# Optimization experiments

Hardware: AMD Instinct MI355X
Metric: run time of the kernel (lower is better)

The kernel has to match this reference:

```python
import jax, jax.numpy as jnp
import numpy as np

B, V, TG = 512, 16, 48
LAB, MED, GLU, E = 256, 192, 16, 64


def _attn_enc(x, W1, b1, Wq, Wk):
    # Attn_encoder: project then self-attend; out [..., L, H]
    h = jnp.tanh(x @ W1 + b1)
    q, k = h @ Wq, h @ Wk
    a = jax.nn.softmax(jnp.einsum('...qd,...kd->...qk', q, k) / jnp.sqrt(jnp.float32(Wq.shape[1])), axis=-1)
    return a @ h


def _mha(q, k, v, Wq, Wk, Wv, Wo, H=4):
    # module's MHA: output length follows v (v acts as query side)
    d = Wq.shape[1]; dh = d // H
    qh = (v @ Wq).reshape(v.shape[:-1] + (H, dh))
    kh = (k @ Wk).reshape(k.shape[:-1] + (H, dh))
    vh = (q @ Wv).reshape(q.shape[:-1] + (H, dh))
    a = jax.nn.softmax(jnp.einsum('...qhd,...khd->...hqk', qh, kh) / jnp.sqrt(jnp.float32(dh)), axis=-1)
    o = jnp.einsum('...hqk,...khd->...qhd', a, vh)
    return o.reshape(o.shape[:-2] + (d,)) @ Wo


def _forward(lab, glu, time, med, ehr_adj, ddi_adj, time_adj,
             Ws1, bs1, Ws2, bs2, Wl1, bl1, Wl2, bl2, Wl3, bl3,
             Wm1, bm1, Wmq, Wmk, Wg1, bg1, Wgq, Wgk,
             gru_Wx, gru_Wh, gru_b,
             m1_Wq, m1_Wk, m1_Wv, m1_Wo, m2_Wq, m2_Wk, m2_Wv, m2_Wo,
             Wo1, bo1, Wo2, bo2):
    Bn, Vn, Tn = glu.shape
    G = gru_Wh.shape[0]
    # static_ll: [B, E//2] repeated over visits
    s = jax.nn.relu(lab @ Ws1 + bs1)
    s = jax.nn.relu(s @ Ws2 + bs2)
    static_fea = jnp.broadcast_to(s[:, None, :], (Bn, Vn, s.shape[-1]))
    # glu_encoder: GRU over per-visit glucose/time readings -> [B, V, GLU]
    x = jnp.stack([glu, time], -1).reshape(Bn * Vn, Tn, 2)
    xs = jnp.swapaxes(x, 0, 1)  # [T, BV, 2]
    def step(h, xt):
        g = xt @ gru_Wx + gru_b
        gh = h @ gru_Wh
        z = jax.nn.sigmoid(g[:, :G] + gh[:, :G])
        r = jax.nn.sigmoid(g[:, G:2 * G] + gh[:, G:2 * G])
        n = jnp.tanh(g[:, 2 * G:] + r * gh[:, 2 * G:])
        return (1.0 - z) * n + z * h, None
    hT, _ = jax.lax.scan(step, jnp.zeros((Bn * Vn, G), glu.dtype), xs)
    glu_enc = hT.reshape(Bn, Vn, G)
    glu_rep = _attn_enc(glu_enc, Wg1, bg1, Wgq, Wgk)        # [B, V, E//2]
    patient_rep = jnp.concatenate([glu_rep, static_fea], -1)  # [B, V, E]
    med_rep = _attn_enc(med[:, :-1, :], Wm1, bm1, Wmq, Wmk)   # [B, V-1, E]
    # drug memory from graph adjacencies (shared across patients)
    drug_mem = (ehr_adj @ Wl1 + bl1) + (time_adj @ Wl2 + bl2) - (ddi_adj @ Wl3 + bl3)  # [MED, E]
    E_en = _mha(patient_rep, patient_rep, med_rep, m1_Wq, m1_Wk, m1_Wv, m1_Wo)  # [B, V-1, E]
    dm = jnp.broadcast_to(drug_mem, (Bn,) + drug_mem.shape)
    E_de = _mha(E_en, E_en, dm, m2_Wq, m2_Wk, m2_Wv, m2_Wo)   # [B, MED, E]
    final = E_de.reshape(Bn, -1)
    o = jax.nn.relu(final)
    o = jax.nn.relu(o @ Wo1 + bo1)
    return o @ Wo2 + bo2  # [B, MED]


def setup_inputs() -> dict:
    ks = iter(jax.random.split(jax.random.key(0), 64))
    def nrm(shape, s=0.05):
        return jax.random.normal(next(ks), shape, dtype=jnp.float32) * s
    z = lambda *shape: jnp.zeros(shape, jnp.float32)
    d = {}
    d['lab'] = jax.random.normal(next(ks), (B, LAB), dtype=jnp.float32)
    d['glu'] = jax.random.normal(next(ks), (B, V, TG), dtype=jnp.float32)
    d['time'] = jax.random.uniform(next(ks), (B, V, TG), dtype=jnp.float32)
    d['med'] = jax.random.uniform(next(ks), (B, V, MED), dtype=jnp.float32)
    d['ehr_adj'] = jax.random.uniform(next(ks), (MED, MED), dtype=jnp.float32)
    d['ddi_adj'] = jax.random.uniform(next(ks), (MED, MED), dtype=jnp.float32)
    d['time_adj'] = jax.random.uniform(next(ks), (MED, MED), dtype=jnp.float32)
    d['Ws1'] = nrm((LAB, E)); d['bs1'] = z(E)
    d['Ws2'] = nrm((E, E // 2)); d['bs2'] = z(E // 2)
    d['Wl1'] = nrm((MED, E)); d['bl1'] = z(E)
    d['Wl2'] = nrm((MED, E)); d['bl2'] = z(E)
    d['Wl3'] = nrm((MED, E)); d['bl3'] = z(E)
    d['Wm1'] = nrm((MED, E)); d['bm1'] = z(E)
    d['Wmq'] = nrm((E, E // 2)); d['Wmk'] = nrm((E, E // 2))
    d['Wg1'] = nrm((GLU, E // 2)); d['bg1'] = z(E // 2)
    d['Wgq'] = nrm((E // 2, E // 4)); d['Wgk'] = nrm((E // 2, E // 4))
    d['gru_Wx'] = nrm((2, 3 * GLU)); d['gru_Wh'] = nrm((GLU, 3 * GLU)); d['gru_b'] = z(3 * GLU)
    for p in ['m1', 'm2']:
        for w in ['Wq', 'Wk', 'Wv', 'Wo']:
            d[p + '_' + w] = nrm((E, E))
    d['Wo1'] = nrm((E * MED, E * MED // 8)); d['bo1'] = z(E * MED // 8)
    d['Wo2'] = nrm((E * MED // 8, MED)); d['bo2'] = z(MED)
    return d


def reference(lab, glu, time, med, ehr_adj, ddi_adj, time_adj,
              Ws1, bs1, Ws2, bs2, Wl1, bl1, Wl2, bl2, Wl3, bl3,
              Wm1, bm1, Wmq, Wmk, Wg1, bg1, Wgq, Wgk,
              gru_Wx, gru_Wh, gru_b,
              m1_Wq, m1_Wk, m1_Wv, m1_Wo, m2_Wq, m2_Wk, m2_Wv, m2_Wo,
              Wo1, bo1, Wo2, bo2):
    return _forward(lab, glu, time, med, ehr_adj, ddi_adj, time_adj,
                    Ws1, bs1, Ws2, bs2, Wl1, bl1, Wl2, bl2, Wl3, bl3,
                    Wm1, bm1, Wmq, Wmk, Wg1, bg1, Wgq, Wgk,
                    gru_Wx, gru_Wh, gru_b,
                    m1_Wq, m1_Wk, m1_Wv, m1_Wo, m2_Wq, m2_Wk, m2_Wv, m2_Wo,
                    Wo1, bo1, Wo2, bo2)
```

## Files before the change

kernel.cpp:

```cpp
#include <hip/hip_runtime.h>
#include <math.h>

#define DEVINL __device__ __forceinline__

DEVINL float sigm(float x) { return 1.0f / (1.0f + __expf(-x)); }
DEVINL float tanh_fast(float x) { return 2.0f / (1.0f + __expf(-2.0f * x)) - 1.0f; }
DEVINL unsigned short bf16rne(float f) {
    unsigned u = __float_as_uint(f);
    return (unsigned short)((u + 0x7FFFu + ((u >> 16) & 1u)) >> 16);
}

typedef __attribute__((ext_vector_type(8))) short bf16x8;
typedef __attribute__((ext_vector_type(4))) float f32x4;

__global__ void gemm_small(const float* __restrict__ A, const float* __restrict__ W,
                           const float* __restrict__ bias, float* __restrict__ C,
                           int M, int N, int K, int act, int vgroup)
{
    int idx = blockIdx.x * blockDim.x + threadIdx.x;
    if (idx >= M * N) return;
    int m = idx / N, n = idx - m * N;
    int am = m;
    if (vgroup) { int g = m / vgroup; am = g * (vgroup + 1) + (m - g * vgroup); }
    const float* a = A + (size_t)am * K;
    const float* w = W + n;
    float acc = bias ? bias[n] : 0.0f;
    for (int k = 0; k < K; k += 4) {
        float4 av = *(const float4*)&a[k];
        float w0 = w[(size_t)k * N];
        float w1 = w[(size_t)(k + 1) * N];
        float w2 = w[(size_t)(k + 2) * N];
        float w3 = w[(size_t)(k + 3) * N];
        acc = fmaf(av.x, w0, acc);
        acc = fmaf(av.y, w1, acc);
        acc = fmaf(av.z, w2, acc);
        acc = fmaf(av.w, w3, acc);
    }
    if (act == 1) acc = fmaxf(acc, 0.0f);
    else if (act == 2) acc = tanh_fast(acc);
    C[idx] = acc;
}

__global__ __launch_bounds__(256) void gru_wave(const float* __restrict__ glu,
    const float* __restrict__ timev, const float* __restrict__ Wx,
    const float* __restrict__ Wh, const float* __restrict__ bb,
    float* __restrict__ out)
{
    __shared__ float sWh[768], sWx[96], sb[48];
    int tid = threadIdx.x;
    for (int i = tid; i < 768; i += 256) sWh[i] = Wh[i];
    if (tid < 96) sWx[tid] = Wx[tid];
    if (tid < 48) sb[tid] = bb[tid];
    __syncthreads();
    int j = tid & 15;
    int seq = blockIdx.x * 16 + (tid >> 4);
    int gbase = (tid & 63) & 0x30;
    float whz[16], whr[16], whn[16];
#pragma unroll
    for (int i = 0; i < 16; ++i) {
        whz[i] = sWh[i * 48 + j];
        whr[i] = sWh[i * 48 + 16 + j];
        whn[i] = sWh[i * 48 + 32 + j];
    }
    float wxz0 = sWx[j],      wxr0 = sWx[16 + j], wxn0 = sWx[32 + j];
    float wxz1 = sWx[48 + j], wxr1 = sWx[64 + j], wxn1 = sWx[80 + j];
    float bz = sb[j], br = sb[16 + j], bn = sb[32 + j];
    const float* gp = glu + (size_t)seq * 48;
    const float* tp = timev + (size_t)seq * 48;
    float h = 0.0f;
    for (int t = 0; t < 48; ++t) {
        float gl = gp[t], tm = tp[t];
        float gz = fmaf(gl, wxz0, fmaf(tm, wxz1, bz));
        float gr = fmaf(gl, wxr0, fmaf(tm, wxr1, br));
        float gn = fmaf(gl, wxn0, fmaf(tm, wxn1, bn));
        float ghn = 0.0f;
#pragma unroll
        for (int i = 0; i < 16; ++i) {
            float hb = __shfl(h, gbase + i, 64);
            gz = fmaf(hb, whz[i], gz);
            gr = fmaf(hb, whr[i], gr);
            ghn = fmaf(hb, whn[i], ghn);
        }
        float z = sigm(gz), r = sigm(gr);
        float n = tanh_fast(gn + r * ghn);
        h = (1.0f - z) * n + z * h;
    }
    out[(size_t)seq * 16 + j] = h;
}

__global__ __launch_bounds__(256) void glu_attn(const float* __restrict__ hg,
    const float* __restrict__ Wq, const float* __restrict__ Wk,
    const float* __restrict__ s2, float* __restrict__ patient)
{
    int b = blockIdx.x, tid = threadIdx.x;
    __shared__ float sh[512], sq[256], sk[256], ss[256];
    sh[tid] = hg[(size_t)b * 512 + tid];
    sh[256 + tid] = hg[(size_t)b * 512 + 256 + tid];
    __syncthreads();
    {
        int p = tid >> 4, j = tid & 15;
        float aq = 0.0f, ak = 0.0f;
        for (int i = 0; i < 32; ++i) {
            float hv = sh[p * 32 + i];
            aq = fmaf(hv, Wq[i * 16 + j], aq);
            ak = fmaf(hv, Wk[i * 16 + j], ak);
        }
        sq[tid] = aq; sk[tid] = ak;
    }
    __syncthreads();
    {
        int p = tid >> 4, pk = tid & 15;
        float a = 0.0f;
        for (int j = 0; j < 16; ++j) a = fmaf(sq[p * 16 + j], sk[pk * 16 + j], a);
        ss[tid] = a * 0.25f;
    }
    __syncthreads();
    if (tid < 16) {
        float mx = -1e30f;
        for (int k = 0; k < 16; ++k) mx = fmaxf(mx, ss[tid * 16 + k]);
        float sum = 0.0f;
        for (int k = 0; k < 16; ++k) { float e = __expf(ss[tid * 16 + k] - mx); ss[tid * 16 + k] = e; sum += e; }
        float inv = 1.0f / sum;
        for (int k = 0; k < 16; ++k) ss[tid * 16 + k] *= inv;
    }
    __syncthreads();
    for (int o = tid; o < 512; o += 256) {
        int p = o >> 5, c = o & 31;
        float acc = 0.0f;
        for (int pk = 0; pk < 16; ++pk) acc = fmaf(ss[p * 16 + pk], sh[pk * 32 + c], acc);
        patient[((size_t)b * 16 + p) * 64 + c] = acc;
        patient[((size_t)b * 16 + p) * 64 + 32 + c] = s2[(size_t)b * 32 + c];
    }
}

__global__ __launch_bounds__(256) void med_attn(const float* __restrict__ hm,
    const float* __restrict__ Wq, const float* __restrict__ Wk,
    float* __restrict__ med_rep)
{
    int b = blockIdx.x, tid = threadIdx.x;
    __shared__ float sh[960], sq[480], sk[480], ss[225];
    for (int i = tid; i < 960; i += 256) sh[i] = hm[(size_t)b * 960 + i];
    __syncthreads();
    for (int o = tid; o < 480; o += 256) {
        int p = o >> 5, j = o & 31;
        float aq = 0.0f, ak = 0.0f;
        for (int i = 0; i < 64; ++i) {
            float hv = sh[p * 64 + i];
            aq = fmaf(hv, Wq[i * 32 + j], aq);
            ak = fmaf(hv, Wk[i * 32 + j], ak);
        }
        sq[o] = aq; sk[o] = ak;
    }
    __syncthreads();
    if (tid < 225) {
        int p = tid / 15, pk = tid - p * 15;
        float a = 0.0f;
        for (int j = 0; j < 32; ++j) a = fmaf(sq[p * 32 + j], sk[pk * 32 + j], a);
        ss[tid] = a * 0.17677669529663687f;
    }
    __syncthreads();
    if (tid < 15) {
        float mx = -1e30f;
        for (int k = 0; k < 15; ++k) mx = fmaxf(mx, ss[tid * 15 + k]);
        float sum = 0.0f;
        for (int k = 0; k < 15; ++k) { float e = __expf(ss[tid * 15 + k] - mx); ss[tid * 15 + k] = e; sum += e; }
        float inv = 1.0f / sum;
        for (int k = 0; k < 15; ++k) ss[tid * 15 + k] *= inv;
    }
    __syncthreads();
    for (int o = tid; o < 960; o += 256) {
        int p = o >> 6, c = o & 63;
        float acc = 0.0f;
        for (int pk = 0; pk < 15; ++pk) acc = fmaf(ss[p * 15 + pk], sh[pk * 64 + c], acc);
        med_rep[(size_t)b * 960 + o] = acc;
    }
}

__global__ void drugmem_kernel(const float* __restrict__ ehr, const float* __restrict__ tadj,
    const float* __restrict__ ddi,
    const float* __restrict__ Wl1, const float* __restrict__ bl1,
    const float* __restrict__ Wl2, const float* __restrict__ bl2,
    const float* __restrict__ Wl3, const float* __restrict__ bl3,
    float* __restrict__ dm)
{
    int idx = blockIdx.x * 256 + threadIdx.x;
    if (idx >= 192 * 64) return;
    int m = idx >> 6, n = idx & 63;
    float acc = bl1[n] + bl2[n] - bl3[n];
    for (int k = 0; k < 192; ++k) {
        acc = fmaf(ehr[m * 192 + k], Wl1[k * 64 + n], acc);
        acc = fmaf(tadj[m * 192 + k], Wl2[k * 64 + n], acc);
        acc = fmaf(-ddi[m * 192 + k], Wl3[k * 64 + n], acc);
    }
    dm[idx] = acc;
}

__global__ __launch_bounds__(256) void mha1_attn(const float* __restrict__ qh1,
    const float* __restrict__ kh1, const float* __restrict__ vh1,
    const float* __restrict__ Wo, float* __restrict__ Een)
{
    int b = blockIdx.x, tid = threadIdx.x;
    __shared__ float sq[1020], sk[1088], sv[1024], ss[960], so[960];
    for (int i = tid; i < 960; i += 256) sq[(i >> 6) * 68 + (i & 63)] = qh1[(size_t)b * 960 + i];
    for (int i = tid; i < 1024; i += 256) {
        sk[(i >> 6) * 68 + (i & 63)] = kh1[(size_t)b * 1024 + i];
        sv[i] = vh1[(size_t)b * 1024 + i];
    }
    __syncthreads();
    for (int o = tid; o < 960; o += 256) {
        int hh = o / 240, rem = o - hh * 240, q = rem >> 4, k = rem & 15;
        float a = 0.0f;
        for (int d = 0; d < 16; ++d) a = fmaf(sq[q * 68 + hh * 16 + d], sk[k * 68 + hh * 16 + d], a);
        ss[o] = a * 0.25f;
    }
    __syncthreads();
    if (tid < 60) {
        int base = tid * 16;
        float mx = -1e30f;
        for (int k = 0; k < 16; ++k) mx = fmaxf(mx, ss[base + k]);
        float sum = 0.0f;
        for (int k = 0; k < 16; ++k) { float e = __expf(ss[base + k] - mx); ss[base + k] = e; sum += e; }
        float inv = 1.0f / sum;
        for (int k = 0; k < 16; ++k) ss[base + k] *= inv;
    }
    __syncthreads();
    for (int o = tid; o < 960; o += 256) {
        int q = o >> 6, j = o & 63, hh = j >> 4;
        float a = 0.0f;
        for (int k = 0; k < 16; ++k) a = fmaf(ss[hh * 240 + q * 16 + k], sv[k * 64 + j], a);
        so[o] = a;
    }
    __syncthreads();
    for (int o = tid; o < 960; o += 256) {
        int q = o >> 6, c = o & 63;
        float a = 0.0f;
        for (int j = 0; j < 64; ++j) a = fmaf(so[q * 64 + j], Wo[j * 64 + c], a);
        Een[(size_t)b * 960 + o] = a;
    }
}

__global__ __launch_bounds__(256) void mha2_attn2(const float* __restrict__ qh2,
    const float* __restrict__ kh2, const float* __restrict__ vh2,
    float* __restrict__ so_all)
{
    int b = blockIdx.x >> 2, q0 = (blockIdx.x & 3) * 48;
    int tid = threadIdx.x;
    __shared__ float skp[1020], sv[960], ss[2880];
    for (int i = tid; i < 960; i += 256) {
        skp[(i >> 6) * 68 + (i & 63)] = kh2[(size_t)b * 960 + i];
        sv[i] = vh2[(size_t)b * 960 + i];
    }
    __syncthreads();
    for (int o = tid; o < 2880; o += 256) {
        int hh = o / 720, rem = o - hh * 720, q = rem / 15, k = rem - q * 15;
        const float* qp = qh2 + (size_t)(q0 + q) * 64 + hh * 16;
        float a = 0.0f;
        for (int d = 0; d < 16; ++d) a = fmaf(qp[d], skp[k * 68 + hh * 16 + d], a);
        ss[o] = a * 0.25f;
    }
    __syncthreads();
    if (tid < 192) {
        int hh = tid / 48, q = tid - hh * 48;
        int base = hh * 720 + q * 15;
        float mx = -1e30f;
        for (int k = 0; k < 15; ++k) mx = fmaxf(mx, ss[base + k]);
        float sum = 0.0f;
        for (int k = 0; k < 15; ++k) { float e = __expf(ss[base + k] - mx); ss[base + k] = e; sum += e; }
        float inv = 1.0f / sum;
        for (int k = 0; k < 15; ++k) ss[base + k] *= inv;
    }
    __syncthreads();
    for (int o = tid; o < 3072; o += 256) {
        int q = o >> 6, j = o & 63, hh = j >> 4;
        float a = 0.0f;
        for (int k = 0; k < 15; ++k) a = fmaf(ss[hh * 720 + q * 15 + k], sv[k * 64 + j], a);
        so_all[((size_t)b * 192 + q0 + q) * 64 + j] = a;
    }
}

__global__ __launch_bounds__(256) void gemm64_relu_bf16(const float* __restrict__ A,
    const float* __restrict__ B, unsigned short* __restrict__ Obf)
{
    __shared__ float As[64 * 20];
    __shared__ float Bs[16 * 64];
    int tid = threadIdx.x;
    int m0 = blockIdx.x * 64;
    float acc[4][4] = {};
    int arow = tid >> 2, akq = (tid & 3) << 2;
    int brow = tid >> 4, bnq = (tid & 15) << 2;
    int tm0 = (tid >> 4) << 2, tn0 = (tid & 15) << 2;
    for (int kt = 0; kt < 64; kt += 16) {
        float4 av = *(const float4*)&A[(size_t)(m0 + arow) * 64 + kt + akq];
        *(float4*)&As[arow * 20 + akq] = av;
        float4 bv = *(const float4*)&B[(size_t)(kt + brow) * 64 + bnq];
        *(float4*)&Bs[brow * 64 + bnq] = bv;
        __syncthreads();
#pragma unroll
        for (int kk = 0; kk < 16; ++kk) {
            float4 b4 = *(const float4*)&Bs[kk * 64 + tn0];
            float a0 = As[(tm0 + 0) * 20 + kk];
            float a1 = As[(tm0 + 1) * 20 + kk];
            float a2 = As[(tm0 + 2) * 20 + kk];
            float a3 = As[(tm0 + 3) * 20 + kk];
            acc[0][0] = fmaf(a0, b4.x, acc[0][0]); acc[0][1] = fmaf(a0, b4.y, acc[0][1]);
            acc[0][2] = fmaf(a0, b4.z, acc[0][2]); acc[0][3] = fmaf(a0, b4.w, acc[0][3]);
            acc[1][0] = fmaf(a1, b4.x, acc[1][0]); acc[1][1] = fmaf(a1, b4.y, acc[1][1]);
            acc[1][2] = fmaf(a1, b4.z, acc[1][2]); acc[1][3] = fmaf(a1, b4.w, acc[1][3]);
            acc[2][0] = fmaf(a2, b4.x, acc[2][0]); acc[2][1] = fmaf(a2, b4.y, acc[2][1]);
            acc[2][2] = fmaf(a2, b4.z, acc[2][2]); acc[2][3] = fmaf(a2, b4.w, acc[2][3]);
            acc[3][0] = fmaf(a3, b4.x, acc[3][0]); acc[3][1] = fmaf(a3, b4.y, acc[3][1]);
            acc[3][2] = fmaf(a3, b4.z, acc[3][2]); acc[3][3] = fmaf(a3, b4.w, acc[3][3]);
        }
        __syncthreads();
    }
#pragma unroll
    for (int i = 0; i < 4; ++i) {
        unsigned r0 = (unsigned)bf16rne(fmaxf(acc[i][0], 0.f)) | ((unsigned)bf16rne(fmaxf(acc[i][1], 0.f)) << 16);
        unsigned r1 = (unsigned)bf16rne(fmaxf(acc[i][2], 0.f)) | ((unsigned)bf16rne(fmaxf(acc[i][3], 0.f)) << 16);
        uint2 v = { r0, r1 };
        *(uint2*)&Obf[(size_t)(m0 + tm0 + i) * 64 + tn0] = v;
    }
}

__global__ __launch_bounds__(256) void gemm_mfma_bf16(
    const unsigned short* __restrict__ Abf, const float* __restrict__ B,
    float* __restrict__ Cp, int M, int N, int K, int klen)
{
    __shared__ unsigned short As[64 * 64];
    __shared__ unsigned short Bs[64 * 64];
    int tid = threadIdx.x;
    int lane = tid & 63, wid = tid >> 6;
    int wr = wid >> 1, wc = wid & 1;
    int n0 = blockIdx.x * 64, m0 = blockIdx.y * 64;
    int kbase0 = blockIdx.z * klen;
    f32x4 acc[2][2] = {};

    int bn = tid & 63, bkc = (tid >> 6) * 16;
    for (int kt = 0; kt < klen; kt += 64) {
        int kb = kbase0 + kt;
#pragma unroll
        for (int c = 0; c < 2; ++c) {
            int ch = tid + c * 256;
            int row = ch >> 3, kc0 = (ch & 7) << 3;
            uint4 v = *(const uint4*)&Abf[(size_t)(m0 + row) * K + kb + kc0];
            int bo = ((row << 7) + (kc0 << 1)) ^ ((row & 7) << 4);
            *(uint4*)((char*)As + bo) = v;
        }
        {
            const float* bp = &B[(size_t)(kb + bkc) * N + n0 + bn];
#pragma unroll
            for (int j = 0; j < 16; j += 2) {
                float f0 = bp[(size_t)j * N];
                float f1 = bp[(size_t)(j + 1) * N];
                unsigned u = (unsigned)bf16rne(f0) | ((unsigned)bf16rne(f1) << 16);
                int k = bkc + j;
                int bo = ((bn << 7) + (k << 1)) ^ ((bn & 7) << 4);
                *(unsigned*)((char*)Bs + bo) = u;
            }
        }
        __syncthreads();
#pragma unroll
        for (int kk = 0; kk < 64; kk += 32) {
            int kb2 = (kk + ((lane >> 4) << 3)) << 1;
            bf16x8 af[2], bfg[2];
#pragma unroll
            for (int fm = 0; fm < 2; ++fm) {
                int row = (wr << 5) + (fm << 4) + (lane & 15);
                af[fm] = *(const bf16x8*)((const char*)As + (((row << 7) + kb2) ^ ((row & 7) << 4)));
            }
#pragma unroll
            for (int fn = 0; fn < 2; ++fn) {
                int col = (wc << 5) + (fn << 4) + (lane & 15);
                bfg[fn] = *(const bf16x8*)((const char*)Bs + (((col << 7) + kb2) ^ ((col & 7) << 4)));
            }
#pragma unroll
            for (int fm = 0; fm < 2; ++fm)
#pragma unroll
                for (int fn = 0; fn < 2; ++fn)
                    acc[fm][fn] = __builtin_amdgcn_mfma_f32_16x16x32_bf16(af[fm], bfg[fn], acc[fm][fn], 0, 0, 0);
        }
        __syncthreads();
    }
    float* cp = Cp + (size_t)blockIdx.z * M * N;
#pragma unroll
    for (int fm = 0; fm < 2; ++fm)
#pragma unroll
        for (int fn = 0; fn < 2; ++fn) {
            int row = m0 + (wr << 5) + (fm << 4) + ((lane >> 4) << 2);
            int col = n0 + (wc << 5) + (fn << 4) + (lane & 15);
#pragma unroll
            for (int r = 0; r < 4; ++r)
                cp[(size_t)(row + r) * N + col] = acc[fm][fn][r];
        }
}

template <int RELU_A>
__global__ __launch_bounds__(256) void gemm_sk(const float* __restrict__ A,
    const float* __restrict__ B, float* __restrict__ Cp,
    int M, int N, int K, int klen)
{
    __shared__ float As[64 * 20];
    __shared__ float Bs[16 * 64];
    int tid = threadIdx.x;
    int n0 = blockIdx.x * 64, m0 = blockIdx.y * 64;
    int bs = blockIdx.z;
    int kbase0 = bs * klen;
    float acc[4][4] = {};
    int arow = tid >> 2, akq = (tid & 3) << 2;
    int brow = tid >> 4, bnq = (tid & 15) << 2;
    int tm0 = (tid >> 4) << 2, tn0 = (tid & 15) << 2;
    for (int kt = 0; kt < klen; kt += 16) {
        int kb = kbase0 + kt;
        float4 av = *(const float4*)&A[(size_t)(m0 + arow) * K + kb + akq];
        if (RELU_A) {
            av.x = fmaxf(av.x, 0.0f); av.y = fmaxf(av.y, 0.0f);
            av.z = fmaxf(av.z, 0.0f); av.w = fmaxf(av.w, 0.0f);
        }
        *(float4*)&As[arow * 20 + akq] = av;
        float4 bv = *(const float4*)&B[(size_t)(kb + brow) * N + n0 + bnq];
        *(float4*)&Bs[brow * 64 + bnq] = bv;
        __syncthreads();
#pragma unroll
        for (int kk = 0; kk < 16; ++kk) {
            float4 b4 = *(const float4*)&Bs[kk * 64 + tn0];
            float a0 = As[(tm0 + 0) * 20 + kk];
            float a1 = As[(tm0 + 1) * 20 + kk];
            float a2 = As[(tm0 + 2) * 20 + kk];
            float a3 = As[(tm0 + 3) * 20 + kk];
            acc[0][0] = fmaf(a0, b4.x, acc[0][0]); acc[0][1] = fmaf(a0, b4.y, acc[0][1]);
            acc[0][2] = fmaf(a0, b4.z, acc[0][2]); acc[0][3] = fmaf(a0, b4.w, acc[0][3]);
            acc[1][0] = fmaf(a1, b4.x, acc[1][0]); acc[1][1] = fmaf(a1, b4.y, acc[1][1]);
            acc[1][2] = fmaf(a1, b4.z, acc[1][2]); acc[1][3] = fmaf(a1, b4.w, acc[1][3]);
            acc[2][0] = fmaf(a2, b4.x, acc[2][0]); acc[2][1] = fmaf(a2, b4.y, acc[2][1]);
            acc[2][2] = fmaf(a2, b4.z, acc[2][2]); acc[2][3] = fmaf(a2, b4.w, acc[2][3]);
            acc[3][0] = fmaf(a3, b4.x, acc[3][0]); acc[3][1] = fmaf(a3, b4.y, acc[3][1]);
            acc[3][2] = fmaf(a3, b4.z, acc[3][2]); acc[3][3] = fmaf(a3, b4.w, acc[3][3]);
        }
        __syncthreads();
    }
    float* cp = Cp + (size_t)bs * M * N;
#pragma unroll
    for (int i = 0; i < 4; ++i)
#pragma unroll
        for (int j = 0; j < 4; ++j)
            cp[(size_t)(m0 + tm0 + i) * N + n0 + tn0 + j] = acc[i][j];
}

__global__ void reduce_bias_act(const float* __restrict__ part, const float* __restrict__ bias,
                                float* __restrict__ out, int MN, int N, int S, int relu)
{
    int idx = blockIdx.x * 256 + threadIdx.x;
    if (idx >= MN) return;
    float a = bias[idx % N];
    for (int s = 0; s < S; ++s) a += part[(size_t)s * MN + idx];
    if (relu) a = fmaxf(a, 0.0f);
    out[idx] = a;
}

extern "C" void kernel_launch(void* const* d_in, const int* in_sizes, int n_in,
                              void* d_out, int out_size, void* d_ws, size_t ws_size,
                              hipStream_t stream)
{
    const float* lab    = (const float*)d_in[0];
    const float* glu    = (const float*)d_in[1];
    const float* timev  = (const float*)d_in[2];
    const float* med    = (const float*)d_in[3];
    const float* ehr    = (const float*)d_in[4];
    const float* ddi    = (const float*)d_in[5];
    const float* tadj   = (const float*)d_in[6];
    const float* Ws1    = (const float*)d_in[7];
    const float* bs1    = (const float*)d_in[8];
    const float* Ws2    = (const float*)d_in[9];
    const float* bs2    = (const float*)d_in[10];
    const float* Wl1    = (const float*)d_in[11];
    const float* bl1    = (const float*)d_in[12];
    const float* Wl2    = (const float*)d_in[13];
    const float* bl2    = (const float*)d_in[14];
    const float* Wl3    = (const float*)d_in[15];
    const float* bl3    = (const float*)d_in[16];
    const float* Wm1    = (const float*)d_in[17];
    const float* bm1    = (const float*)d_in[18];
    const float* Wmq    = (const float*)d_in[19];
    const float* Wmk    = (const float*)d_in[20];
    const float* Wg1    = (const float*)d_in[21];
    const float* bg1    = (const float*)d_in[22];
    const float* Wgq    = (const float*)d_in[23];
    const float* Wgk    = (const float*)d_in[24];
    const float* gWx    = (const float*)d_in[25];
    const float* gWh    = (const float*)d_in[26];
    const float* gb     = (const float*)d_in[27];
    const float* m1Wq   = (const float*)d_in[28];
    const float* m1Wk   = (const float*)d_in[29];
    const float* m1Wv   = (const float*)d_in[30];
    const float* m1Wo   = (const float*)d_in[31];
    const float* m2Wq   = (const float*)d_in[32];
    const float* m2Wk   = (const float*)d_in[33];
    const float* m2Wv   = (const float*)d_in[34];
    const float* m2Wo   = (const float*)d_in[35];
    const float* Wo1    = (const float*)d_in[36];
    const float* bo1    = (const float*)d_in[37];
    const float* Wo2    = (const float*)d_in[38];
    const float* bo2    = (const float*)d_in[39];

    float* W = (float*)d_ws;
    size_t off = 0;
    auto alloc = [&](size_t n) { size_t r = off; off += (n + 3) & ~(size_t)3; return r; };
    size_t o_s1      = alloc(512 * 64);
    size_t o_s2      = alloc(512 * 32);
    size_t o_gluenc  = alloc(8192 * 16);
    size_t o_hg      = alloc(8192 * 32);
    size_t o_patient = alloc(8192 * 64);
    size_t o_medh    = alloc(7680 * 64);
    size_t o_medrep  = alloc(7680 * 64);
    size_t o_dm      = alloc(192 * 64);
    size_t o_qh2s    = alloc(192 * 64);
    size_t o_qh1     = alloc(7680 * 64);
    size_t o_kh1     = alloc(8192 * 64);
    size_t o_vh1     = alloc(8192 * 64);
    size_t o_Een     = alloc(7680 * 64);
    size_t o_kh2 = o_medh;
    size_t o_vh2 = o_qh1;
    size_t o_abf = 0;
    size_t o_so      = alloc((size_t)512 * 12288);
    size_t o_h1      = alloc((size_t)512 * 1536);
    size_t o_part    = o_so;

    {
        dim3 g(1, 8, 4);
        gemm_sk<0><<<g, 256, 0, stream>>>(lab, Ws1, W + o_part, 512, 64, 256, 64);
        reduce_bias_act<<<128, 256, 0, stream>>>(W + o_part, bs1, W + o_s1, 512 * 64, 64, 4, 1);
    }
    gemm_small<<<64, 256, 0, stream>>>(W + o_s1, Ws2, bs2, W + o_s2, 512, 32, 64, 1, 0);
    gru_wave<<<512, 256, 0, stream>>>(glu, timev, gWx, gWh, gb, W + o_gluenc);
    gemm_small<<<1024, 256, 0, stream>>>(W + o_gluenc, Wg1, bg1, W + o_hg, 8192, 32, 16, 2, 0);
    glu_attn<<<512, 256, 0, stream>>>(W + o_hg, Wgq, Wgk, W + o_s2, W + o_patient);
    gemm_small<<<1920, 256, 0, stream>>>(med, Wm1, bm1, W + o_medh, 7680, 64, 192, 2, 15);
    med_attn<<<512, 256, 0, stream>>>(W + o_medh, Wmq, Wmk, W + o_medrep);
    drugmem_kernel<<<48, 256, 0, stream>>>(ehr, tadj, ddi, Wl1, bl1, Wl2, bl2, Wl3, bl3, W + o_dm);
    gemm_small<<<48, 256, 0, stream>>>(W + o_dm, m2Wq, nullptr, W + o_qh2s, 192, 64, 64, 0, 0);
    gemm_small<<<1920, 256, 0, stream>>>(W + o_medrep, m1Wq, nullptr, W + o_qh1, 7680, 64, 64, 0, 0);
    gemm_small<<<2048, 256, 0, stream>>>(W + o_patient, m1Wk, nullptr, W + o_kh1, 8192, 64, 64, 0, 0);
    gemm_small<<<2048, 256, 0, stream>>>(W + o_patient, m1Wv, nullptr, W + o_vh1, 8192, 64, 64, 0, 0);
    mha1_attn<<<512, 256, 0, stream>>>(W + o_qh1, W + o_kh1, W + o_vh1, m1Wo, W + o_Een);
    gemm_small<<<1920, 256, 0, stream>>>(W + o_Een, m2Wk, nullptr, W + o_kh2, 7680, 64, 64, 0, 0);
    gemm_small<<<1920, 256, 0, stream>>>(W + o_Een, m2Wv, nullptr, W + o_vh2, 7680, 64, 64, 0, 0);
    mha2_attn2<<<2048, 256, 0, stream>>>(W + o_qh2s, W + o_kh2, W + o_vh2, W + o_so);
    gemm64_relu_bf16<<<1536, 256, 0, stream>>>(W + o_so, m2Wo, (unsigned short*)(W + o_abf));
    {
        dim3 g(24, 8, 4);
        gemm_mfma_bf16<<<g, 256, 0, stream>>>((const unsigned short*)(W + o_abf), Wo1,
                                              W + o_part, 512, 1536, 12288, 3072);
        reduce_bias_act<<<3072, 256, 0, stream>>>(W + o_part, bo1, W + o_h1, 512 * 1536, 1536, 4, 1);
    }
    {
        dim3 g(3, 8, 16);
        gemm_sk<0><<<g, 256, 0, stream>>>(W + o_h1, Wo2, W + o_part, 512, 192, 1536, 96);
        reduce_bias_act<<<384, 256, 0, stream>>>(W + o_part, bo2, (float*)d_out, 512 * 192, 192, 16, 0);
    }
}
```

Measured before the change: 277.1 us.

## Enlarge MFMA GEMM M-tile to 128, double split-K, fuse K/V projections

Two separate small GEMMs that read the same input for the K and V projections are merged into one dual-output kernel, so the activation is read once and there is one launch fewer per pair. The large bf16 MFMA GEMM now uses a 128x64 block tile, with each wave covering 32 rows by all 64 columns, which improves reuse of each B tile loaded into shared memory. Split-K goes from 4 to 8 slices to keep the grid size the same. The trade-off is more partial-sum traffic into the reduction, plus higher LDS and register use per block.

After: 254.7 us (median of 4 runs). -8.1%, faster.

```diff
diff --git a/kernel.cpp b/kernel.cpp
--- a/kernel.cpp
+++ b/kernel.cpp
@@ -41,6 +41,32 @@
     C[idx] = acc;
 }
 
+__global__ void gemm_small_dual(const float* __restrict__ A,
+    const float* __restrict__ W1, const float* __restrict__ W2,
+    float* __restrict__ C1, float* __restrict__ C2, int M, int N, int K)
+{
+    int idx = blockIdx.x * blockDim.x + threadIdx.x;
+    if (idx >= M * N) return;
+    int m = idx / N, n = idx - m * N;
+    const float* a = A + (size_t)m * K;
+    const float* w1 = W1 + n;
+    const float* w2 = W2 + n;
+    float acc1 = 0.0f, acc2 = 0.0f;
+    for (int k = 0; k < K; k += 4) {
+        float4 av = *(const float4*)&a[k];
+        float p0 = w1[(size_t)k * N],       q0 = w2[(size_t)k * N];
+        float p1 = w1[(size_t)(k + 1) * N], q1 = w2[(size_t)(k + 1) * N];
+        float p2 = w1[(size_t)(k + 2) * N], q2 = w2[(size_t)(k + 2) * N];
+        float p3 = w1[(size_t)(k + 3) * N], q3 = w2[(size_t)(k + 3) * N];
+        acc1 = fmaf(av.x, p0, acc1); acc2 = fmaf(av.x, q0, acc2);
+        acc1 = fmaf(av.y, p1, acc1); acc2 = fmaf(av.y, q1, acc2);
+        acc1 = fmaf(av.z, p2, acc1); acc2 = fmaf(av.z, q2, acc2);
+        acc1 = fmaf(av.w, p3, acc1); acc2 = fmaf(av.w, q3, acc2);
+    }
+    C1[idx] = acc1;
+    C2[idx] = acc2;
+}
+
 __global__ __launch_bounds__(256) void gru_wave(const float* __restrict__ glu,
     const float* __restrict__ timev, const float* __restrict__ Wx,
     const float* __restrict__ Wh, const float* __restrict__ bb,
@@ -326,20 +352,19 @@
     const unsigned short* __restrict__ Abf, const float* __restrict__ B,
     float* __restrict__ Cp, int M, int N, int K, int klen)
 {
-    __shared__ unsigned short As[64 * 64];
+    __shared__ unsigned short As[128 * 64];
     __shared__ unsigned short Bs[64 * 64];
     int tid = threadIdx.x;
-    int lane = tid & 63, wid = tid >> 6;
-    int wr = wid >> 1, wc = wid & 1;
-    int n0 = blockIdx.x * 64, m0 = blockIdx.y * 64;
+    int lane = tid & 63, w = tid >> 6;
+    int n0 = blockIdx.x * 64, m0 = blockIdx.y * 128;
     int kbase0 = blockIdx.z * klen;
-    f32x4 acc[2][2] = {};
+    f32x4 acc[2][4] = {};
 
     int bn = tid & 63, bkc = (tid >> 6) * 16;
     for (int kt = 0; kt < klen; kt += 64) {
         int kb = kbase0 + kt;
 #pragma unroll
-        for (int c = 0; c < 2; ++c) {
+        for (int c = 0; c < 4; ++c) {
             int ch = tid + c * 256;
             int row = ch >> 3, kc0 = (ch & 7) << 3;
             uint4 v = *(const uint4*)&Abf[(size_t)(m0 + row) * K + kb + kc0];
@@ -362,21 +387,21 @@
 #pragma unroll
         for (int kk = 0; kk < 64; kk += 32) {
             int kb2 = (kk + ((lane >> 4) << 3)) << 1;
-            bf16x8 af[2], bfg[2];
+            bf16x8 af[2], bfg[4];
 #pragma unroll
             for (int fm = 0; fm < 2; ++fm) {
-                int row = (wr << 5) + (fm << 4) + (lane & 15);
+                int row = (w << 5) + (fm << 4) + (lane & 15);
                 af[fm] = *(const bf16x8*)((const char*)As + (((row << 7) + kb2) ^ ((row & 7) << 4)));
             }
 #pragma unroll
-            for (int fn = 0; fn < 2; ++fn) {
-                int col = (wc << 5) + (fn << 4) + (lane & 15);
+            for (int fn = 0; fn < 4; ++fn) {
+                int col = (fn << 4) + (lane & 15);
                 bfg[fn] = *(const bf16x8*)((const char*)Bs + (((col << 7) + kb2) ^ ((col & 7) << 4)));
             }
 #pragma unroll
             for (int fm = 0; fm < 2; ++fm)
 #pragma unroll
-                for (int fn = 0; fn < 2; ++fn)
+                for (int fn = 0; fn < 4; ++fn)
                     acc[fm][fn] = __builtin_amdgcn_mfma_f32_16x16x32_bf16(af[fm], bfg[fn], acc[fm][fn], 0, 0, 0);
         }
         __syncthreads();
@@ -385,9 +410,9 @@
 #pragma unroll
     for (int fm = 0; fm < 2; ++fm)
 #pragma unroll
-        for (int fn = 0; fn < 2; ++fn) {
-            int row = m0 + (wr << 5) + (fm << 4) + ((lane >> 4) << 2);
-            int col = n0 + (wc << 5) + (fn << 4) + (lane & 15);
+        for (int fn = 0; fn < 4; ++fn) {
+            int row = m0 + (w << 5) + (fm << 4) + ((lane >> 4) << 2);
+            int col = n0 + (fn << 4) + (lane & 15);
 #pragma unroll
             for (int r = 0; r < 4; ++r)
                 cp[(size_t)(row + r) * N + col] = acc[fm][fn][r];
@@ -539,18 +564,18 @@
     drugmem_kernel<<<48, 256, 0, stream>>>(ehr, tadj, ddi, Wl1, bl1, Wl2, bl2, Wl3, bl3, W + o_dm);
     gemm_small<<<48, 256, 0, stream>>>(W + o_dm, m2Wq, nullptr, W + o_qh2s, 192, 64, 64, 0, 0);
     gemm_small<<<1920, 256, 0, stream>>>(W + o_medrep, m1Wq, nullptr, W + o_qh1, 7680, 64, 64, 0, 0);
-    gemm_small<<<2048, 256, 0, stream>>>(W + o_patient, m1Wk, nullptr, W + o_kh1, 8192, 64, 64, 0, 0);
-    gemm_small<<<2048, 256, 0, stream>>>(W + o_patient, m1Wv, nullptr, W + o_vh1, 8192, 64, 64, 0, 0);
+    gemm_small_dual<<<2048, 256, 0, stream>>>(W + o_patient, m1Wk, m1Wv,
+                                              W + o_kh1, W + o_vh1, 8192, 64, 64);
     mha1_attn<<<512, 256, 0, stream>>>(W + o_qh1, W + o_kh1, W + o_vh1, m1Wo, W + o_Een);
-    gemm_small<<<1920, 256, 0, stream>>>(W + o_Een, m2Wk, nullptr, W + o_kh2, 7680, 64, 64, 0, 0);
-    gemm_small<<<1920, 256, 0, stream>>>(W + o_Een, m2Wv, nullptr, W + o_vh2, 7680, 64, 64, 0, 0);
+    gemm_small_dual<<<1920, 256, 0, stream>>>(W + o_Een, m2Wk, m2Wv,
+                                              W + o_kh2, W + o_vh2, 7680, 64, 64);
     mha2_attn2<<<2048, 256, 0, stream>>>(W + o_qh2s, W + o_kh2, W + o_vh2, W + o_so);
     gemm64_relu_bf16<<<1536, 256, 0, stream>>>(W + o_so, m2Wo, (unsigned short*)(W + o_abf));
     {
-        dim3 g(24, 8, 4);
+        dim3 g(24, 4, 8);
         gemm_mfma_bf16<<<g, 256, 0, stream>>>((const unsigned short*)(W + o_abf), Wo1,
-                                              W + o_part, 512, 1536, 12288, 3072);
-        reduce_bias_act<<<3072, 256, 0, stream>>>(W + o_part, bo1, W + o_h1, 512 * 1536, 1536, 4, 1);
+                                              W + o_part, 512, 1536, 12288, 1536);
+        reduce_bias_act<<<3072, 256, 0, stream>>>(W + o_part, bo1, W + o_h1, 512 * 1536, 1536, 8, 1);
     }
     {
         dim3 g(3, 8, 16);
```
